# Optimization experiments

Measured on AMD Instinct MI355X. Metric: run time of the kernel, lower is better.

The kernel has to match this reference:

```python
import jax, jax.numpy as jnp
import numpy as np

STRIDE = 16
RATIOS = (0.5, 1.0, 2.0)
SCALES = (8, 16, 32)
NMS_THRESH = 0.7
NUM_PRE = 12000
NUM_POST = 2000
MIN_SIZE = 16.0


def _all_anchors(feat_h, feat_w):
    # base anchors centered at (stride/2, stride/2), (y1, x1, y2, x2)
    base = []
    for r in RATIOS:
        for s in SCALES:
            h = STRIDE * s * np.sqrt(r)
            w = STRIDE * s * np.sqrt(1.0 / r)
            c = STRIDE / 2.0
            base.append([c - h / 2.0, c - w / 2.0, c + h / 2.0, c + w / 2.0])
    base = np.asarray(base, np.float32)  # (A, 4)
    ys = np.arange(feat_h, dtype=np.float32) * STRIDE
    xs = np.arange(feat_w, dtype=np.float32) * STRIDE
    shift = np.stack(np.meshgrid(ys, xs, indexing='ij'), axis=-1)  # (H, W, 2) = (y, x)
    shift4 = np.concatenate([shift, shift], axis=-1)  # (H, W, 4)
    anchors = shift4[:, :, None, :] + base[None, None, :, :]  # (H, W, A, 4)
    return jnp.asarray(anchors.reshape(-1, 4))


def _conv(x, w, b, padding):
    y = jax.lax.conv_general_dilated(x, w, (1, 1), padding,
                                     dimension_numbers=('NCHW', 'OIHW', 'NCHW'))
    return y + b[None, :, None, None]


def _create_rpn_proposals(locs, scores, anchors, img_h, img_w):
    # box deparameterize (y1,x1,y2,x2 anchors; dy,dx,dh,dw locs)
    ha = anchors[:, 2] - anchors[:, 0]
    wa = anchors[:, 3] - anchors[:, 1]
    cya = anchors[:, 0] + 0.5 * ha
    cxa = anchors[:, 1] + 0.5 * wa
    cy = locs[:, 0] * ha + cya
    cx = locs[:, 1] * wa + cxa
    h = ha * jnp.exp(locs[:, 2])
    w = wa * jnp.exp(locs[:, 3])
    boxes = jnp.stack([cy - 0.5 * h, cx - 0.5 * w, cy + 0.5 * h, cx + 0.5 * w], axis=1)

    order = jnp.argsort(-scores)[:NUM_PRE]
    boxes = boxes[order]
    s = scores[order]

    lim = jnp.array([img_h, img_w, img_h, img_w], dtype=boxes.dtype)
    boxes = jnp.clip(boxes, 0.0, lim)
    valid = ((boxes[:, 2] - boxes[:, 0]) >= MIN_SIZE) & ((boxes[:, 3] - boxes[:, 1]) >= MIN_SIZE)

    areas = (boxes[:, 2] - boxes[:, 0]) * (boxes[:, 3] - boxes[:, 1])
    n = boxes.shape[0]
    idx = jnp.arange(n)

    def body(i, suppressed):
        bi = boxes[i]
        yy1 = jnp.maximum(bi[0], boxes[:, 0])
        xx1 = jnp.maximum(bi[1], boxes[:, 1])
        yy2 = jnp.minimum(bi[2], boxes[:, 2])
        xx2 = jnp.minimum(bi[3], boxes[:, 3])
        inter = jnp.maximum(yy2 - yy1, 0.0) * jnp.maximum(xx2 - xx1, 0.0)
        iou = inter / (areas[i] + areas - inter + 1e-10)
        new_sup = suppressed | ((iou > NMS_THRESH) & (idx > i))
        return jnp.where(suppressed[i], suppressed, new_sup)

    suppressed = jax.lax.fori_loop(0, n, body, ~valid)
    keep = (~suppressed) & valid
    rank = jnp.cumsum(keep) - 1
    tgt = jnp.where(keep & (rank < NUM_POST), rank, NUM_POST)  # overflow slot
    out = jnp.zeros((NUM_POST + 1, 4), boxes.dtype).at[tgt].set(boxes)[:NUM_POST]
    return out  # (2000, 4), zero-padded if fewer kept


def setup_inputs() -> dict:
    key = jax.random.key(0)
    ks = jax.random.split(key, 7)
    in_c, out_c, A = 1024, 512, 9
    x = jax.random.normal(ks[0], (1, in_c, 64, 64), dtype=jnp.float32)
    conv_w = jax.random.normal(ks[1], (out_c, in_c, 3, 3), jnp.float32) * 0.01
    conv_b = jnp.zeros((out_c,), jnp.float32)
    score_w = jax.random.normal(ks[2], (A * 2, out_c, 1, 1), jnp.float32) * 0.01
    score_b = jnp.zeros((A * 2,), jnp.float32)
    loc_w = jax.random.normal(ks[3], (A * 4, out_c, 1, 1), jnp.float32) * 0.01
    loc_b = jnp.zeros((A * 4,), jnp.float32)
    return {"x": x, "conv_w": conv_w, "conv_b": conv_b,
            "score_w": score_w, "score_b": score_b,
            "loc_w": loc_w, "loc_b": loc_b,
            "img_h": 1024, "img_w": 1024}


def reference(x, conv_w, conv_b, score_w, score_b, loc_w, loc_b, img_h, img_w):
    _, _, fh, fw = x.shape
    anchors = _all_anchors(fh, fw)  # (fh*fw*A, 4)
    h = jax.nn.leaky_relu(_conv(x, conv_w, conv_b, 'SAME'), 0.01)
    rpn_locs = _conv(h, loc_w, loc_b, 'VALID').transpose(0, 2, 3, 1).reshape(-1, 4)
    rpn_scores = _conv(h, score_w, score_b, 'VALID').transpose(0, 2, 3, 1).reshape(-1, 2)
    fg = jax.nn.softmax(rpn_scores, axis=1)[:, 1]
    rois = _create_rpn_proposals(jax.lax.stop_gradient(rpn_locs),
                                 jax.lax.stop_gradient(fg),
                                 anchors, img_h, img_w)
    return rpn_locs, rpn_scores, rois, anchors
```

## Files before the change

kernel.cpp:

```cpp
#include <hip/hip_runtime.h>
#include <cstdint>
#include <cstddef>
#include <math.h>

#define NANCH    36864
#define NPRE     12000
#define NPRE_PAD 12032
#define NW       188
#define SORT_N   16384
#define NPOST    2000

typedef double d4_t __attribute__((ext_vector_type(4)));

__device__ __forceinline__ int tribase(int ci) { return ci * NW - (ci * (ci - 1)) / 2; }

typedef __attribute__((address_space(1))) const void* as1cv_t;
typedef __attribute__((address_space(3))) void* as3v_t;
__device__ __forceinline__ void gload_lds16(const float* g, float* l)
{
    __builtin_amdgcn_global_load_lds((as1cv_t)g, (as3v_t)l, 16, 0, 0);
}

__global__ __launch_bounds__(256, 2)
void k_conv_mfma(const float* __restrict__ xg, const float* __restrict__ wg_,
                 const float* __restrict__ bg, float* __restrict__ hg)
{
    __shared__ __align__(16) float wlds[3][4608];
    __shared__ __align__(16) float xlds[3][1632];
    const int tid = threadIdx.x;
    const int oct = blockIdx.x & 7;
    const int y   = blockIdx.x >> 3;
    const int oc0 = oct << 6;
    const int l   = tid & 63;
    const int wv  = tid >> 6;
    const int g   = l >> 4;
    const int li  = l & 15;
    const int wm  = wv >> 1;
    const int wn  = wv & 1;
    const int slot5 = 16 + (wv & 1);

    int pr[4], qc[4];
    int aG = g;
    {
        d4_t Pz = {0., 0., 0., 0.}, Qz = {0., 0., 0., 0.}, Tz = {0., 0., 0., 0.};
        Pz = __builtin_amdgcn_mfma_f64_16x16x4f64((double)li, 1.0, Pz, 0, 0, 0);
        Qz = __builtin_amdgcn_mfma_f64_16x16x4f64(1.0, (double)li, Qz, 0, 0, 0);
        Tz = __builtin_amdgcn_mfma_f64_16x16x4f64((double)g, (double)(1 << (2 * g)),
                                                  Tz, 0, 0, 0);
        bool ok = true;
        const int tval = (int)Tz[0];
        if ((int)Tz[1] != tval || (int)Tz[2] != tval || (int)Tz[3] != tval) ok = false;
        int seen = 0;
#pragma unroll
        for (int j = 0; j < 4; ++j) {
            int d = (tval >> (2 * j)) & 3;
            seen |= 1 << d;
            if (d == g) aG = j;
        }
        if (seen != 15) ok = false;
#pragma unroll
        for (int r = 0; r < 4; ++r) {
            int pv = (int)Pz[r], qv = (int)Qz[r];
            if ((pv & 3) || (qv & 3)) ok = false;
            pr[r] = pv >> 2; qc[r] = qv >> 2;
            if (pr[r] > 15 || qc[r] > 15) ok = false;
        }
        if (!ok) {
#pragma unroll
            for (int r = 0; r < 4; ++r) { pr[r] = 4 * g + r; qc[r] = li; }
            aG = g;
        }
    }

    d4_t acc00 = {0., 0., 0., 0.}, acc01 = {0., 0., 0., 0.};
    d4_t acc10 = {0., 0., 0., 0.}, acc11 = {0., 0., 0., 0.};

    int xoff[7], loff[7];
#pragma unroll
    for (int t = 0; t < 7; ++t) {
        int f = tid + 256 * t;
        if (f < 1584) {
            int ic = f / 198; int r = f - ic * 198; int sr = r / 66; int gc = r - sr * 66;
            loff[t] = (ic * 3 + sr) * 68 + gc;
            int gy = y + sr - 1, gx = gc - 1;
            xoff[t] = (gy >= 0 && gy < 64 && gx >= 0 && gx < 64)
                      ? (ic * 4096 + gy * 64 + gx) : -1;
        } else { loff[t] = -1; xoff[t] = -1; }
    }
    int xoffL[7];
#pragma unroll
    for (int t = 0; t < 7; ++t) xoffL[t] = (xoff[t] >= 0) ? xoff[t] : 0;

    const float* wsrc0 = wg_ + (size_t)(oc0 + l) * 9216;
    const int abase = wm * 32 + li;
    const int bbase = (wn * 32 + li) * 4 + g;
    float xr[7];

    {
#pragma unroll
        for (int i = 0; i < 4; ++i)
            gload_lds16(wsrc0 + 4 * (wv + 4 * i), &wlds[0][(wv + 4 * i) * 256]);
        gload_lds16(wsrc0 + 4 * slot5, &wlds[0][slot5 * 256]);
#pragma unroll
        for (int t = 0; t < 7; ++t) xr[t] = xg[xoffL[t]];
#pragma unroll
        for (int t = 0; t < 7; ++t)
            if (loff[t] >= 0) xlds[0][loff[t]] = (xoff[t] >= 0) ? xr[t] : 0.f;
        const float* xp = xg + 32768;
#pragma unroll
        for (int t = 0; t < 7; ++t) xr[t] = xp[xoffL[t]];
        asm volatile("s_waitcnt lgkmcnt(0)" ::: "memory");
        asm volatile("s_waitcnt vmcnt(0)" ::: "memory");
        __builtin_amdgcn_sched_barrier(0);
        __builtin_amdgcn_s_barrier();
        __builtin_amdgcn_sched_barrier(0);
    }

    int cur = 0;
#pragma unroll 1
    for (int cc = 0; cc < 128; ++cc) {
        int nxt = cur + 1; if (nxt == 3) nxt = 0;
        if (cc < 127) {
            const float* wsrc = wsrc0 + (cc + 1) * 72;
            float* wdst = &wlds[nxt][0];
#pragma unroll
            for (int i = 0; i < 4; ++i)
                gload_lds16(wsrc + 4 * (wv + 4 * i), wdst + (wv + 4 * i) * 256);
            gload_lds16(wsrc + 4 * slot5, wdst + slot5 * 256);
            __builtin_amdgcn_sched_barrier(0);
            float* xdst = &xlds[nxt][0];
#pragma unroll
            for (int t = 0; t < 7; ++t)
                if (loff[t] >= 0) xdst[loff[t]] = (xoff[t] >= 0) ? xr[t] : 0.f;
            __builtin_amdgcn_sched_barrier(0);
            {
                int nc = (cc + 2 < 128) ? (cc + 2) : 127;
                const float* xp = xg + (size_t)nc * 32768;
#pragma unroll
                for (int t = 0; t < 7; ++t) xr[t] = xp[xoffL[t]];
            }
            __builtin_amdgcn_sched_barrier(0);
            asm volatile("s_waitcnt lgkmcnt(0)" ::: "memory");
            asm volatile("s_waitcnt vmcnt(12)" ::: "memory");
        } else {
            asm volatile("s_waitcnt lgkmcnt(0)" ::: "memory");
            asm volatile("s_waitcnt vmcnt(0)" ::: "memory");
        }
        __builtin_amdgcn_sched_barrier(0);
        __builtin_amdgcn_s_barrier();
        __builtin_amdgcn_sched_barrier(0);

        const float* wb = &wlds[cur][0];
        const float* xb = &xlds[cur][0];
        __builtin_amdgcn_s_setprio(1);
#pragma unroll
        for (int s = 0; s < 18; ++s) {
            int k   = 4 * s + aG;
            int icL = k / 9; int tap = k - 9 * icL;
            int ky  = tap / 3; int kx = tap - 3 * ky;
            int ax  = (icL * 3 + ky) * 68 + kx + abase;
            double a0 = (double)xb[ax];
            double a1 = (double)xb[ax + 16];
            double b0 = (double)wb[bbase + s * 256];
            double b1 = (double)wb[bbase + s * 256 + 64];
            acc00 = __builtin_amdgcn_mfma_f64_16x16x4f64(a0, b0, acc00, 0, 0, 0);
            acc01 = __builtin_amdgcn_mfma_f64_16x16x4f64(a0, b1, acc01, 0, 0, 0);
            acc10 = __builtin_amdgcn_mfma_f64_16x16x4f64(a1, b0, acc10, 0, 0, 0);
            acc11 = __builtin_amdgcn_mfma_f64_16x16x4f64(a1, b1, acc11, 0, 0, 0);
        }
        __builtin_amdgcn_s_setprio(0);
        cur = nxt;
    }

    __syncthreads();
    float* olds = &wlds[0][0];
    {
#pragma unroll
        for (int r = 0; r < 4; ++r) {
            const int oca = wn * 32 + qc[r];
            const int ocb = oca + 16;
            const double ba = (double)bg[oc0 + oca];
            const double bb = (double)bg[oc0 + ocb];
            const int pxa = wm * 32 + pr[r];
            const int pxb = pxa + 16;
            double t00 = acc00[r] + ba;
            double t01 = acc01[r] + bb;
            double t10 = acc10[r] + ba;
            double t11 = acc11[r] + bb;
            olds[oca * 68 + pxa] = (float)((t00 >= 0.0) ? t00 : 0.01 * t00);
            olds[ocb * 68 + pxa] = (float)((t01 >= 0.0) ? t01 : 0.01 * t01);
            olds[oca * 68 + pxb] = (float)((t10 >= 0.0) ? t10 : 0.01 * t10);
            olds[ocb * 68 + pxb] = (float)((t11 >= 0.0) ? t11 : 0.01 * t11);
        }
    }
    __syncthreads();
    {
        const int oc = tid >> 2, q = tid & 3;
        float* dst = hg + (size_t)(oc0 + oc) * 4096 + y * 64 + q * 16;
        const float* src = &olds[oc * 68 + q * 16];
#pragma unroll
        for (int j = 0; j < 4; ++j)
            *(float4*)(dst + 4 * j) = *(const float4*)(src + 4 * j);
    }
}

__global__ __launch_bounds__(256, 1)
void k_heads(const float* __restrict__ hg, const float* __restrict__ loc_w,
             const float* __restrict__ loc_b, const float* __restrict__ score_w,
             const float* __restrict__ score_b, const int* __restrict__ imh,
             const int* __restrict__ imw, float* __restrict__ out,
             float* __restrict__ boxes_all, unsigned long long* __restrict__ keys64)
{
    __shared__ float  hch[64 * 64];
    __shared__ float  wch[54 * 64];
    __shared__ float  ol[54 * 64];
    __shared__ double sld[18 * 64];
    const int y = blockIdx.x, tid = threadIdx.x;
    const int px = tid & 63, cg = tid >> 6;
    double acc[14];
#pragma unroll
    for (int u = 0; u < 14; ++u) acc[u] = 0.0;
    for (int cc = 0; cc < 8; ++cc) {
        __syncthreads();
#pragma unroll
        for (int t = 0; t < 16; ++t) {
            int f = tid + 256 * t;
            hch[f] = hg[(size_t)(cc * 64 + (f >> 6)) * 4096 + y * 64 + (f & 63)];
        }
#pragma unroll
        for (int t = 0; t < 14; ++t) {
            int f = tid + 256 * t;
            if (f < 54 * 64) {
                int ch = f >> 6, c = f & 63;
                wch[f] = (ch < 36) ? loc_w[ch * 512 + cc * 64 + c]
                                   : score_w[(ch - 36) * 512 + cc * 64 + c];
            }
        }
        __syncthreads();
        for (int c = 0; c < 64; ++c) {
            double hvd = (double)hch[c * 64 + px];
#pragma unroll
            for (int u = 0; u < 14; ++u) {
                int ch = cg + 4 * u;
                if (ch < 54) acc[u] = fma((double)wch[ch * 64 + c], hvd, acc[u]);
            }
        }
    }
    __syncthreads();
#pragma unroll
    for (int u = 0; u < 14; ++u) {
        int ch = cg + 4 * u;
        if (ch < 54) {
            double s = acc[u] + (double)((ch < 36) ? loc_b[ch] : score_b[ch - 36]);
            ol[ch * 64 + px] = (float)s;
            if (ch >= 36) sld[(ch - 36) * 64 + px] = s;
        }
    }
    __syncthreads();
    for (int f = tid; f < 64 * 36; f += 256) {
        int p = f / 36, ch = f - 36 * p;
        out[(size_t)(y * 64 + p) * 36 + ch] = ol[ch * 64 + p];
    }
    for (int f = tid; f < 64 * 18; f += 256) {
        int p = f / 18, ch = f - 18 * p;
        out[147456 + (size_t)(y * 64 + p) * 18 + ch] = ol[(36 + ch) * 64 + p];
    }
    const float fy = (float)(*imh), fx = (float)(*imw);
    float* anch = out + 229184;
    for (int t2 = tid; t2 < 576; t2 += 256) {
        int p = t2 / 9, a = t2 - 9 * p;
        int pg = y * 64 + p;
        int ar = a / 3, as = a - 3 * ar;
        double rr = (ar == 0) ? 0.5 : ((ar == 1) ? 1.0 : 2.0);
        double ss = (as == 0) ? 8.0 : ((as == 1) ? 16.0 : 32.0);
        double hh = 16.0 * ss * sqrt(rr), wwd = 16.0 * ss * sqrt(1.0 / rr);
        float by1 = (float)(8.0 - hh * 0.5), bx1 = (float)(8.0 - wwd * 0.5);
        float by2 = (float)(8.0 + hh * 0.5), bx2 = (float)(8.0 + wwd * 0.5);
        float sy = (float)(y * 16), sx = (float)(p * 16);
        float a0 = sy + by1, a1 = sx + bx1, a2 = sy + by2, a3 = sx + bx2;
        int base = (pg * 9 + a) * 4;
        anch[base + 0] = a0; anch[base + 1] = a1; anch[base + 2] = a2; anch[base + 3] = a3;
        double d = sld[(a * 2 + 1) * 64 + p] - sld[(a * 2) * 64 + p];
        long long bits = __double_as_longlong(d);
        unsigned long long u64 =
            (unsigned long long)(bits ^ ((bits >> 63) | (long long)0x8000000000000000LL));
        unsigned long long v = ~u64;
        keys64[pg * 9 + a] = (v & 0xFFFFFFFFFFFF0000ULL) | (unsigned long long)(pg * 9 + a);
        float dy = ol[(a * 4 + 0) * 64 + p], dxv = ol[(a * 4 + 1) * 64 + p];
        float dh = ol[(a * 4 + 2) * 64 + p], dwv = ol[(a * 4 + 3) * 64 + p];
        float hA = a2 - a0, wA = a3 - a1;
        float cya = a0 + 0.5f * hA, cxa = a1 + 0.5f * wA;
        float cy = dy * hA + cya, cx = dxv * wA + cxa;
        float hb = hA * expf(dh), wb = wA * expf(dwv);
        float b0 = fminf(fmaxf(cy - 0.5f * hb, 0.f), fy);
        float b1 = fminf(fmaxf(cx - 0.5f * wb, 0.f), fx);
        float b2 = fminf(fmaxf(cy + 0.5f * hb, 0.f), fy);
        float b3 = fminf(fmaxf(cx + 0.5f * wb, 0.f), fx);
        boxes_all[base + 0] = b0; boxes_all[base + 1] = b1;
        boxes_all[base + 2] = b2; boxes_all[base + 3] = b3;
    }
}

__global__ __launch_bounds__(1024, 1)
void k_select(const unsigned long long* __restrict__ keys64,
              const float* __restrict__ boxes_all,
              unsigned long long* __restrict__ sortbuf, float* __restrict__ sbox,
              float* __restrict__ areas, unsigned long long* __restrict__ suppr)
{
    __shared__ unsigned int hist[256];
    __shared__ unsigned int sh_below, sh_prefix, sh_nsel;
    __shared__ unsigned long long tile[4096];
    const int tid = threadIdx.x;
    if (tid == 0) { sh_below = 0; sh_prefix = 0; sh_nsel = 0; }
    __syncthreads();
    for (int p = 3; p >= 0; --p) {
        if (tid < 256) hist[tid] = 0;
        __syncthreads();
        unsigned int pref = sh_prefix;
        int shift = p * 8;
        for (int i = tid; i < NANCH; i += 1024) {
            unsigned int k = (unsigned int)(keys64[i] >> 32);
            bool match = (p == 3) || ((k >> (shift + 8)) == pref);
            if (match) atomicAdd(&hist[(k >> shift) & 255u], 1u);
        }
        __syncthreads();
        if (tid == 0) {
            unsigned int below = sh_below, cacc = 0;
            int b = 0;
            for (; b < 256; ++b) {
                if (below + cacc + hist[b] >= NPRE) break;
                cacc += hist[b];
            }
            if (b > 255) b = 255;
            sh_below = below + cacc;
            sh_prefix = (pref << 8) | (unsigned int)b;
        }
        __syncthreads();
    }
    const unsigned int P = sh_prefix;
    for (int i = tid; i < NANCH; i += 1024) {
        unsigned long long k = keys64[i];
        if ((unsigned int)(k >> 32) <= P) {
            unsigned int pos = atomicAdd(&sh_nsel, 1u);
            if (pos < SORT_N) sortbuf[pos] = k;
        }
    }
    __syncthreads();
    unsigned int nsel = sh_nsel; if (nsel > SORT_N) nsel = SORT_N;
    for (unsigned int i = nsel + tid; i < SORT_N; i += 1024) sortbuf[i] = ~0ULL;
    __syncthreads();
    for (int T = 0; T < 4; ++T) {
        for (int t = tid; t < 4096; t += 1024) tile[t] = sortbuf[T * 4096 + t];
        __syncthreads();
        for (int k2 = 2; k2 <= 4096; k2 <<= 1) {
            for (int j = k2 >> 1; j > 0; j >>= 1) {
                for (int t = tid; t < 2048; t += 1024) {
                    int i = ((t & ~(j - 1)) << 1) | (t & (j - 1));
                    int ip = i | j;
                    bool up = (((T * 4096 + i) & k2) == 0);
                    unsigned long long A = tile[i], B = tile[ip];
                    if ((A > B) == up) { tile[i] = B; tile[ip] = A; }
                }
                __syncthreads();
            }
        }
        for (int t = tid; t < 4096; t += 1024) sortbuf[T * 4096 + t] = tile[t];
        __syncthreads();
    }
    auto gstage = [&](int k2, int j) {
        for (int t = tid; t < 8192; t += 1024) {
            int i = ((t & ~(j - 1)) << 1) | (t & (j - 1));
            int ip = i | j;
            bool up = ((i & k2) == 0);
            unsigned long long A = sortbuf[i], B = sortbuf[ip];
            if ((A > B) == up) { sortbuf[i] = B; sortbuf[ip] = A; }
        }
        __syncthreads();
    };
    auto ltail = [&](int k2) {
        for (int T = 0; T < 4; ++T) {
            for (int t = tid; t < 4096; t += 1024) tile[t] = sortbuf[T * 4096 + t];
            __syncthreads();
            for (int j = 2048; j > 0; j >>= 1) {
                for (int t = tid; t < 2048; t += 1024) {
                    int i = ((t & ~(j - 1)) << 1) | (t & (j - 1));
                    int ip = i | j;
                    bool up = (((T * 4096 + i) & k2) == 0);
                    unsigned long long A = tile[i], B = tile[ip];
                    if ((A > B) == up) { tile[i] = B; tile[ip] = A; }
                }
                __syncthreads();
            }
            for (int t = tid; t < 4096; t += 1024) sortbuf[T * 4096 + t] = tile[t];
            __syncthreads();
        }
    };
    gstage(8192, 4096);  ltail(8192);
    gstage(16384, 8192); gstage(16384, 4096); ltail(16384);

    if (tid < NW) suppr[tid] = (tid == NW - 1) ? 0xFFFFFFFF00000000ULL : 0ULL;
    __syncthreads();
    for (int r = tid; r < NPRE_PAD; r += 1024) {
        float b0 = 0, b1 = 0, b2 = 0, b3 = 0;
        if (r < NPRE) {
            unsigned int idx = (unsigned int)(sortbuf[r] & 0xFFFFULL);
            const float* bp = boxes_all + (size_t)idx * 4;
            b0 = bp[0]; b1 = bp[1]; b2 = bp[2]; b3 = bp[3];
        }
        sbox[r * 4 + 0] = b0; sbox[r * 4 + 1] = b1;
        sbox[r * 4 + 2] = b2; sbox[r * 4 + 3] = b3;
        areas[r] = (b2 - b0) * (b3 - b1);
        if (r < NPRE) {
            bool valid = ((b2 - b0) >= 16.0f) && ((b3 - b1) >= 16.0f);
            if (!valid) atomicOr(&suppr[r >> 6], 1ULL << (r & 63));
        }
    }
}

__global__ __launch_bounds__(256, 1)
void k_mask(const float* __restrict__ sbox, const float* __restrict__ areas,
            unsigned long long* __restrict__ mask)
{
    const int cj = blockIdx.x, q = blockIdx.y;
    __shared__ float4 bx[64];
    __shared__ float aj[64];
    const int t = threadIdx.x;
    const int j0 = cj * 64;
    if (t < 64) { bx[t] = ((const float4*)sbox)[j0 + t]; aj[t] = areas[j0 + t]; }
    __syncthreads();
    const int c0 = ((cj + 1) * q) >> 2, c1 = ((cj + 1) * (q + 1)) >> 2;
    for (int i0 = c0 * 64; i0 < c1 * 64; i0 += 256) {
        int i = i0 + t;
        if (i < c1 * 64) {
            const float4 p = ((const float4*)sbox)[i];
            const float ai = areas[i];
            unsigned long long w = 0;
            for (int jj = 0; jj < 64; ++jj) {
                float4 qb = bx[jj];
                float yy1 = fmaxf(p.x, qb.x), xx1 = fmaxf(p.y, qb.y);
                float yy2 = fminf(p.z, qb.z), xx2 = fminf(p.w, qb.w);
                float inter = fmaxf(yy2 - yy1, 0.f) * fmaxf(xx2 - xx1, 0.f);
                float iou = inter / (ai + aj[jj] - inter + 1e-10f);
                w |= ((unsigned long long)((iou > 0.7f) && (j0 + jj > i))) << jj;
            }
            int ci = i >> 6;
            mask[(size_t)(tribase(ci) + (cj - ci)) * 64 + (i & 63)] = w;
        }
    }
}

__global__ __launch_bounds__(256, 1)
void k_scan(const unsigned long long* __restrict__ mask,
            const unsigned long long* __restrict__ suppr,
            const float* __restrict__ sbox, float* __restrict__ rois)
{
    __shared__ unsigned long long rvs[NW];
    __shared__ unsigned long long curw;
    __shared__ unsigned long long keptw[NW];
    __shared__ unsigned long long diagbuf[2][64];
    __shared__ int totkept, brk;
    __shared__ int pref[NW + 1];
    const int tid = threadIdx.x;
    if (tid < NW) { rvs[tid] = suppr[tid]; keptw[tid] = 0ULL; }
    if (tid == 0) { totkept = 0; brk = 0; }
    if (tid < 64) diagbuf[0][tid] = mask[tid];
    __syncthreads();
    for (int c = 0; c < NW; ++c) {
        unsigned long long pf = 0;
        const bool isPf = (tid >= 64 && tid < 128 && c + 1 < NW);
        if (isPf) pf = mask[((size_t)tribase(c + 1)) * 64 + (tid - 64)];
        if (tid < 64) {
            unsigned long long diag = diagbuf[c & 1][tid];
            unsigned long long w = rvs[c];
            for (int b = 0; b < 64; ++b) {
                unsigned long long db = __shfl(diag, b, 64);
                if (!((w >> b) & 1ULL)) w |= db;
            }
            if (tid == 0) {
                curw = w;
                keptw[c] = ~w;
                totkept += __popcll(~w);
                if (totkept >= NPOST) brk = 1;
            }
        }
        __syncthreads();
        if (brk) break;
        unsigned long long kw = ~curw;
        if (kw && tid > c && tid < NW) {
            const unsigned long long* mrow = mask + (size_t)(tribase(c) + (tid - c)) * 64;
            unsigned long long acc = 0;
            while (kw) {
                unsigned long long m0 = 0, m1 = 0, m2 = 0, m3 = 0,
                                   m4 = 0, m5 = 0, m6 = 0, m7 = 0;
                int b = (int)__builtin_ctzll(kw); m0 = mrow[b]; kw &= kw - 1;
                if (kw) { b = (int)__builtin_ctzll(kw); m1 = mrow[b]; kw &= kw - 1; }
                if (kw) { b = (int)__builtin_ctzll(kw); m2 = mrow[b]; kw &= kw - 1; }
                if (kw) { b = (int)__builtin_ctzll(kw); m3 = mrow[b]; kw &= kw - 1; }
                if (kw) { b = (int)__builtin_ctzll(kw); m4 = mrow[b]; kw &= kw - 1; }
                if (kw) { b = (int)__builtin_ctzll(kw); m5 = mrow[b]; kw &= kw - 1; }
                if (kw) { b = (int)__builtin_ctzll(kw); m6 = mrow[b]; kw &= kw - 1; }
                if (kw) { b = (int)__builtin_ctzll(kw); m7 = mrow[b]; kw &= kw - 1; }
                acc |= ((m0 | m1) | (m2 | m3)) | ((m4 | m5) | (m6 | m7));
            }
            rvs[tid] |= acc;
        }
        if (isPf) diagbuf[(c + 1) & 1][tid - 64] = pf;
        __syncthreads();
    }
    __syncthreads();
    if (tid == 0) {
        int s = 0;
        for (int c = 0; c < NW; ++c) { pref[c] = s; s += __popcll(keptw[c]); }
        pref[NW] = s;
    }
    __syncthreads();
    int total = pref[NW]; if (total > NPOST) total = NPOST;
    for (int r = total * 4 + tid; r < NPOST * 4; r += 256) rois[r] = 0.f;
    if (tid < NW) {
        unsigned long long kw = keptw[tid];
        int r = pref[tid];
        for (int b = 0; b < 64; ++b) {
            if ((kw >> b) & 1ULL) {
                if (r < NPOST) {
                    const float* bp = sbox + (size_t)(tid * 64 + b) * 4;
                    rois[r * 4 + 0] = bp[0]; rois[r * 4 + 1] = bp[1];
                    rois[r * 4 + 2] = bp[2]; rois[r * 4 + 3] = bp[3];
                }
                ++r;
            }
        }
    }
}

extern "C" void kernel_launch(void* const* d_in, const int* in_sizes, int n_in,
                              void* d_out, int out_size, void* d_ws, size_t ws_size,
                              hipStream_t stream)
{
    const float* x       = (const float*)d_in[0];
    const float* conv_w  = (const float*)d_in[1];
    const float* conv_b  = (const float*)d_in[2];
    const float* score_w = (const float*)d_in[3];
    const float* score_b = (const float*)d_in[4];
    const float* loc_w   = (const float*)d_in[5];
    const float* loc_b   = (const float*)d_in[6];
    const int*   imh     = (const int*)d_in[7];
    const int*   imw     = (const int*)d_in[8];
    float* out = (float*)d_out;
    char* ws = (char*)d_ws;
    float* h                    = (float*)(ws);
    float* boxes_all            = (float*)(ws + 8388608);
    unsigned long long* keys64  = (unsigned long long*)(ws + 8978432);
    float* sbox                 = (float*)(ws + 9273344);
    float* areas                = (float*)(ws + 9465856);
    unsigned long long* suppr   = (unsigned long long*)(ws + 9513984);
    unsigned long long* sortbuf = (unsigned long long*)(ws + 9515520);
    unsigned long long* mask    = (unsigned long long*)(ws + 9646592);

    k_conv_mfma<<<512, 256, 0, stream>>>(x, conv_w, conv_b, h);
    k_heads <<<64, 256, 0, stream>>>(h, loc_w, loc_b, score_w, score_b, imh, imw,
                                     out, boxes_all, keys64);
    k_select<<<1, 1024, 0, stream>>>(keys64, boxes_all, sortbuf, sbox, areas, suppr);
    k_mask  <<<dim3(188, 4), 256, 0, stream>>>(sbox, areas, mask);
    k_scan  <<<1, 256, 0, stream>>>(mask, suppr, sbox, out + 221184);
}
```

Baseline: 1.706 ms.

## Deepen conv prefetch to two stages and preload first MFMA operands

Restructures the triple-buffered LDS pipeline in the FP64-MFMA conv kernel so weights and inputs are prefetched two chunks ahead instead of one. The first k-step's LDS operands for the next chunk are loaded at the end of the current iteration, which hides LDS latency at the start of the MFMA loop. Some intermediate waitcnts and sched barriers are removed, and a second barrier per iteration is added. This relies on fine-grained lgkmcnt/vmcnt counting, which is fragile, and the extra barrier adds sync cost.

```diff
diff --git a/kernel.cpp b/kernel.cpp
--- a/kernel.cpp
+++ b/kernel.cpp
@@ -94,7 +94,10 @@
     const float* wsrc0 = wg_ + (size_t)(oc0 + l) * 9216;
     const int abase = wm * 32 + li;
     const int bbase = (wn * 32 + li) * 4 + g;
+    const int ax0   = (aG / 3) * 68 + (aG - 3 * (aG / 3)) + abase;
     float xr[7];
+    float fa0, fa1, fb0, fb1;
+    double pa0, pa1, pb0, pb1;
 
     {
 #pragma unroll
@@ -102,59 +105,72 @@
             gload_lds16(wsrc0 + 4 * (wv + 4 * i), &wlds[0][(wv + 4 * i) * 256]);
         gload_lds16(wsrc0 + 4 * slot5, &wlds[0][slot5 * 256]);
 #pragma unroll
+        for (int i = 0; i < 4; ++i)
+            gload_lds16(wsrc0 + 72 + 4 * (wv + 4 * i), &wlds[1][(wv + 4 * i) * 256]);
+        gload_lds16(wsrc0 + 72 + 4 * slot5, &wlds[1][slot5 * 256]);
+#pragma unroll
         for (int t = 0; t < 7; ++t) xr[t] = xg[xoffL[t]];
 #pragma unroll
         for (int t = 0; t < 7; ++t)
             if (loff[t] >= 0) xlds[0][loff[t]] = (xoff[t] >= 0) ? xr[t] : 0.f;
-        const float* xp = xg + 32768;
-#pragma unroll
-        for (int t = 0; t < 7; ++t) xr[t] = xp[xoffL[t]];
+        {
+            const float* xp = xg + 32768;
+#pragma unroll
+            for (int t = 0; t < 7; ++t) xr[t] = xp[xoffL[t]];
+#pragma unroll
+            for (int t = 0; t < 7; ++t)
+                if (loff[t] >= 0) xlds[1][loff[t]] = (xoff[t] >= 0) ? xr[t] : 0.f;
+        }
+        {
+            const float* xp = xg + 2 * 32768;
+#pragma unroll
+            for (int t = 0; t < 7; ++t) xr[t] = xp[xoffL[t]];
+        }
         asm volatile("s_waitcnt lgkmcnt(0)" ::: "memory");
-        asm volatile("s_waitcnt vmcnt(0)" ::: "memory");
-        __builtin_amdgcn_sched_barrier(0);
+        asm volatile("s_waitcnt vmcnt(7)" ::: "memory");
         __builtin_amdgcn_s_barrier();
-        __builtin_amdgcn_sched_barrier(0);
-    }
-
-    int cur = 0;
+        fa0 = xlds[0][ax0]; fa1 = xlds[0][ax0 + 16];
+        fb0 = wlds[0][bbase]; fb1 = wlds[0][bbase + 64];
+        asm volatile("s_waitcnt lgkmcnt(0)" ::: "memory");
+        pa0 = (double)fa0; pa1 = (double)fa1; pb0 = (double)fb0; pb1 = (double)fb1;
+    }
+
 #pragma unroll 1
     for (int cc = 0; cc < 128; ++cc) {
-        int nxt = cur + 1; if (nxt == 3) nxt = 0;
-        if (cc < 127) {
-            const float* wsrc = wsrc0 + (cc + 1) * 72;
-            float* wdst = &wlds[nxt][0];
+        int cb = cc % 3, nb = (cc + 1) % 3, sb = (cc + 2) % 3;
+        if (cc + 2 < 128) {
+            const float* wsrc = wsrc0 + (cc + 2) * 72;
+            float* wdst = &wlds[sb][0];
 #pragma unroll
             for (int i = 0; i < 4; ++i)
                 gload_lds16(wsrc + 4 * (wv + 4 * i), wdst + (wv + 4 * i) * 256);
             gload_lds16(wsrc + 4 * slot5, wdst + slot5 * 256);
-            __builtin_amdgcn_sched_barrier(0);
-            float* xdst = &xlds[nxt][0];
+            float* xdst = &xlds[sb][0];
 #pragma unroll
             for (int t = 0; t < 7; ++t)
                 if (loff[t] >= 0) xdst[loff[t]] = (xoff[t] >= 0) ? xr[t] : 0.f;
-            __builtin_amdgcn_sched_barrier(0);
             {
-                int nc = (cc + 2 < 128) ? (cc + 2) : 127;
+                int nc = (cc + 3 < 128) ? (cc + 3) : 127;
                 const float* xp = xg + (size_t)nc * 32768;
 #pragma unroll
                 for (int t = 0; t < 7; ++t) xr[t] = xp[xoffL[t]];
             }
-            __builtin_amdgcn_sched_barrier(0);
-            asm volatile("s_waitcnt lgkmcnt(0)" ::: "memory");
             asm volatile("s_waitcnt vmcnt(12)" ::: "memory");
         } else {
-            asm volatile("s_waitcnt lgkmcnt(0)" ::: "memory");
             asm volatile("s_waitcnt vmcnt(0)" ::: "memory");
         }
-        __builtin_amdgcn_sched_barrier(0);
         __builtin_amdgcn_s_barrier();
         __builtin_amdgcn_sched_barrier(0);
 
-        const float* wb = &wlds[cur][0];
-        const float* xb = &xlds[cur][0];
+        const float* wb = &wlds[cb][0];
+        const float* xb = &xlds[cb][0];
         __builtin_amdgcn_s_setprio(1);
-#pragma unroll
-        for (int s = 0; s < 18; ++s) {
+        acc00 = __builtin_amdgcn_mfma_f64_16x16x4f64(pa0, pb0, acc00, 0, 0, 0);
+        acc01 = __builtin_amdgcn_mfma_f64_16x16x4f64(pa0, pb1, acc01, 0, 0, 0);
+        acc10 = __builtin_amdgcn_mfma_f64_16x16x4f64(pa1, pb0, acc10, 0, 0, 0);
+        acc11 = __builtin_amdgcn_mfma_f64_16x16x4f64(pa1, pb1, acc11, 0, 0, 0);
+#pragma unroll
+        for (int s = 1; s < 18; ++s) {
             int k   = 4 * s + aG;
             int icL = k / 9; int tap = k - 9 * icL;
             int ky  = tap / 3; int kx = tap - 3 * ky;
@@ -169,7 +185,19 @@
             acc11 = __builtin_amdgcn_mfma_f64_16x16x4f64(a1, b1, acc11, 0, 0, 0);
         }
         __builtin_amdgcn_s_setprio(0);
-        cur = nxt;
+        __builtin_amdgcn_sched_barrier(0);
+
+        if (cc < 127) {
+            fa0 = xlds[nb][ax0]; fa1 = xlds[nb][ax0 + 16];
+            fb0 = wlds[nb][bbase]; fb1 = wlds[nb][bbase + 64];
+            asm volatile("s_waitcnt lgkmcnt(4)" ::: "memory");
+            __builtin_amdgcn_s_barrier();
+            asm volatile("s_waitcnt lgkmcnt(0)" ::: "memory");
+            pa0 = (double)fa0; pa1 = (double)fa1; pb0 = (double)fb0; pb1 = (double)fb1;
+        } else {
+            asm volatile("s_waitcnt lgkmcnt(0)" ::: "memory");
+            __builtin_amdgcn_s_barrier();
+        }
     }
 
     __syncthreads();
```

Measured after the change: 1.702 ms, median of 2. No clear change (-0.2%).
